# Kernel tuning notes

Hardware: AMD Instinct MI355X
Metric: run time of the kernel (lower is better)

Reference implementation:

```python
import jax, jax.numpy as jnp
import numpy as np

K = 3       # kernel size
PAD = 1     # dcn_pad
STRIDE = 1
DIL = 1     # dilation
GN_EPS = 1e-5


def _conv2d(x, w, b):
    # standard NCHW conv, stride 1, pad 1
    y = jax.lax.conv_general_dilated(
        x, w, (STRIDE, STRIDE), [(PAD, PAD), (PAD, PAD)],
        rhs_dilation=(DIL, DIL),
        dimension_numbers=('NCHW', 'OIHW', 'NCHW'))
    return y + b[None, :, None, None]


def _modulated_deform_conv(x, w_off, b_off, w, b):
    B, C, H, W = x.shape
    KK = K * K
    # offset/mask branch (ModulatedDeformConv2dPack.conv_offset)
    off = _conv2d(x, w_off, b_off)                     # [B, 3*KK, H, W]
    o1, o2, m = jnp.split(off, 3, axis=1)
    offset = jnp.concatenate([o1, o2], axis=1)         # [B, 2*KK, H, W]
    mask = jax.nn.sigmoid(m)                           # [B, KK, H, W]
    # channel 2k = dy, channel 2k+1 = dx for kernel tap k
    offset = offset.reshape(B, KK, 2, H, W)
    dy, dx = offset[:, :, 0], offset[:, :, 1]          # [B, KK, H, W]

    ki = jnp.arange(KK) // K                            # kernel row index
    kj = jnp.arange(KK) % K                             # kernel col index
    base_y = (jnp.arange(H)[None, :, None] - PAD + ki[:, None, None] * DIL)  # [KK,H,1]
    base_x = (jnp.arange(W)[None, None, :] - PAD + kj[:, None, None] * DIL)  # [KK,1,W]
    py = base_y.astype(x.dtype) + dy                   # [B, KK, H, W]
    px = base_x.astype(x.dtype) + dx

    y0f = jnp.floor(py); x0f = jnp.floor(px)
    ly = py - y0f; lx = px - x0f
    y0 = y0f.astype(jnp.int32); x0 = x0f.astype(jnp.int32)

    xf = x.reshape(B, C, H * W)

    def gather(yi, xi):
        # zero-padded gather at integer corner (yi, xi)
        valid = (yi >= 0) & (yi < H) & (xi >= 0) & (xi < W)
        idx = jnp.clip(yi, 0, H - 1) * W + jnp.clip(xi, 0, W - 1)  # [B,KK,H,W]
        g = jax.vmap(lambda xb, ib: jnp.take(xb, ib.reshape(-1), axis=1))(xf, idx)
        g = g.reshape(B, C, KK, H, W)
        return g * valid[:, None].astype(x.dtype)

    val = (gather(y0, x0)         * ((1 - ly) * (1 - lx))[:, None]
         + gather(y0, x0 + 1)     * ((1 - ly) * lx)[:, None]
         + gather(y0 + 1, x0)     * (ly * (1 - lx))[:, None]
         + gather(y0 + 1, x0 + 1) * (ly * lx)[:, None])     # [B,C,KK,H,W]
    val = val * mask[:, None]                                # modulation

    out = jnp.einsum('bckhw,ock->bohw', val, w.reshape(w.shape[0], C, KK))
    return out + b[None, :, None, None]


def _groupnorm1_relu(y, gamma, beta):
    # GroupNorm(num_groups=1): normalize over (C,H,W) per sample
    mu = y.mean(axis=(1, 2, 3), keepdims=True)
    var = y.var(axis=(1, 2, 3), keepdims=True)
    yn = (y - mu) * jax.lax.rsqrt(var + GN_EPS)
    return jax.nn.relu(yn * gamma[None, :, None, None] + beta[None, :, None, None])


def setup_inputs() -> dict:
    key = jax.random.key(0)
    ks = jax.random.split(key, 5)
    B, C, H, W = 4, 256, 64, 64
    CO = 256
    x = jax.random.normal(ks[0], (B, C, H, W), jnp.float32)
    w_off = jax.random.normal(ks[1], (3 * K * K, C, K, K), jnp.float32) * 0.01
    b_off = jax.random.normal(ks[2], (3 * K * K,), jnp.float32) * 0.01
    w = jax.random.normal(ks[3], (CO, C, K, K), jnp.float32) * (1.0 / np.sqrt(C * K * K))
    b = jax.random.normal(ks[4], (CO,), jnp.float32) * 0.01
    gamma = jnp.ones((CO,), jnp.float32)
    beta = jnp.zeros((CO,), jnp.float32)
    return dict(x=x, w_off=w_off, b_off=b_off, w=w, b=b, gamma=gamma, beta=beta)


def reference(x, w_off, b_off, w, b, gamma, beta):
    y = _modulated_deform_conv(x, w_off, b_off, w, b)
    return _groupnorm1_relu(y, gamma, beta)
```

## Files before the change

kernel.cpp:

```cpp
#include <hip/hip_runtime.h>

#define B_ 4
#define C_ 256
#define H_ 64
#define W_ 64
#define HW_ 4096
#define CO_ 256
#define NPX_ 16384
#define GN_EPS_ 1e-5f

typedef float f32x4 __attribute__((ext_vector_type(4)));
typedef short s16x8 __attribute__((ext_vector_type(8)));

__device__ __forceinline__ short f2bf(float f) {
    union { float f; unsigned u; } v; v.f = f;
    unsigned r = (v.u + 0x7FFFu + ((v.u >> 16) & 1u)) >> 16;
    return (short)(r & 0xFFFFu);
}
__device__ __forceinline__ float bf2f(short s) {
    union { unsigned u; float f; } v; v.u = ((unsigned)s & 0xFFFFu) << 16;
    return v.f;
}

__device__ __forceinline__ void gld_lds16(const void* g, void* l) {
    __builtin_amdgcn_global_load_lds(
        (const __attribute__((address_space(1))) unsigned*)g,
        (__attribute__((address_space(3))) unsigned*)l,
        16, 0, 0);
}

__global__ void k_prep_w(const float* __restrict__ w, short* __restrict__ wT) {
    int oc = blockIdx.x, c = threadIdx.x;
    const float* src = w + (oc * 256 + c) * 9;
    float v[9];
#pragma unroll
    for (int t = 0; t < 9; ++t) v[t] = src[t];
#pragma unroll
    for (int t = 0; t < 9; ++t) wT[(t * 256 + oc) * 256 + c] = f2bf(v[t]);
}

__global__ void k_prep_woff(const float* __restrict__ w_off, short* __restrict__ wOffT) {
    int o = blockIdx.x;
    int c = threadIdx.x;
    if (o < 27) {
        const float* src = w_off + (o * 256 + c) * 9;
#pragma unroll
        for (int t = 0; t < 9; ++t)
            wOffT[(t * 32 + o) * 256 + c] = f2bf(src[t]);
    } else {
#pragma unroll
        for (int t = 0; t < 9; ++t)
            wOffT[(t * 32 + o) * 256 + c] = 0;
    }
}

__global__ void k_xpose(const float* __restrict__ x, short* __restrict__ xT) {
    __shared__ short T[64 * 72];

    int bx  = blockIdx.x;
    int px0 = (bx & 255) * 64;
    int c0  = (bx >> 8) * 64;
    int b   = px0 >> 12;
    int hw0 = px0 & 4095;

    int t  = threadIdx.x;
    int cl = t & 63;
    int q  = t >> 6;

    const float4* src = reinterpret_cast<const float4*>(
        x + (long)(b * 256 + c0 + cl) * 4096 + hw0);
#pragma unroll
    for (int j = 0; j < 4; ++j) {
        float4 v = src[j * 4 + q];
        int pl = (j * 4 + q) * 4;
        T[(pl + 0) * 72 + cl] = f2bf(v.x);
        T[(pl + 1) * 72 + cl] = f2bf(v.y);
        T[(pl + 2) * 72 + cl] = f2bf(v.z);
        T[(pl + 3) * 72 + cl] = f2bf(v.w);
    }
    __syncthreads();

    int pl = t >> 2;
    int s  = t & 3;
    short* dst = xT + (long)(px0 + pl) * 256 + c0 + s * 16;
    s16x8 a    = *reinterpret_cast<const s16x8*>(&T[pl * 72 + s * 16]);
    s16x8 bseg = *reinterpret_cast<const s16x8*>(&T[pl * 72 + s * 16 + 8]);
    *reinterpret_cast<s16x8*>(dst)     = a;
    *reinterpret_cast<s16x8*>(dst + 8) = bseg;
}

__global__ __launch_bounds__(256, 4) void k_offmfma(
        const short* __restrict__ xT, const short* __restrict__ wOffT,
        const float* __restrict__ b_off, float* __restrict__ off) {
    int tid  = threadIdx.x;
    int lane = tid & 63;
    int wv   = tid >> 6;

    int px0  = blockIdx.x * 64 + wv * 16;
    int lm   = lane & 15;
    int lk   = (lane >> 4) * 8;

    int pxA = px0 + lm;
    int h   = (pxA >> 6) & 63;
    int w   = pxA & 63;

    f32x4 acc[2];
    acc[0] = (f32x4)0.f; acc[1] = (f32x4)0.f;

#pragma unroll
    for (int kk = 0; kk < 9; ++kk) {
        const int ki = kk / 3, kj = kk % 3;
        int hh = h + ki - 1, ww = w + kj - 1;
        bool valid = ((unsigned)hh < 64u) & ((unsigned)ww < 64u);
        int srcpx = valid ? (pxA + (ki - 1) * 64 + (kj - 1)) : 0;
        const short* aP = xT + (long)srcpx * 256 + lk;
        const short* bP = wOffT + (long)(kk * 32 + lm) * 256 + lk;
#pragma unroll
        for (int ks = 0; ks < 8; ++ks) {
            s16x8 a = *reinterpret_cast<const s16x8*>(aP + ks * 32);
            if (!valid) a = (s16x8)0;
            s16x8 b0 = *reinterpret_cast<const s16x8*>(bP + ks * 32);
            s16x8 b1 = *reinterpret_cast<const s16x8*>(bP + 16 * 256 + ks * 32);
            acc[0] = __builtin_amdgcn_mfma_f32_16x16x32_bf16(a, b0, acc[0], 0, 0, 0);
            acc[1] = __builtin_amdgcn_mfma_f32_16x16x32_bf16(a, b1, acc[1], 0, 0, 0);
        }
    }

#pragma unroll
    for (int nt = 0; nt < 2; ++nt) {
        int oc = nt * 16 + lm;
        if (oc < 27) {
            float bv = b_off[oc];
#pragma unroll
            for (int j = 0; j < 4; ++j) {
                int px = px0 + (lane >> 4) * 4 + j;
                off[oc * NPX_ + px] = acc[nt][j] + bv;
            }
        }
    }
}

__global__ void k_sample(const short* __restrict__ xT, const float* __restrict__ off,
                         short* __restrict__ val) {
    int tid = threadIdx.x;
    int l32 = tid & 31;
    int pxi = tid >> 5;
    int px0 = blockIdx.x * 32;

    int cb = l32 >> 2;
    int cw = (l32 & 3) * 8;

#pragma unroll 1
    for (int kk = 0; kk < 9; ++kk) {
        int ki = kk / 3, kj = kk % 3;
#pragma unroll 1
        for (int it = 0; it < 4; ++it) {
            int p  = px0 + it * 8 + pxi;
            int b  = p >> 12;
            int hw = p & 4095;
            int h  = hw >> 6;
            int wc = hw & 63;

            float dy = off[(2 * kk) * NPX_ + p];
            float dx = off[(2 * kk + 1) * NPX_ + p];
            float mk = off[(18 + kk) * NPX_ + p];
            mk = 1.f / (1.f + __expf(-mk));

            float py  = (float)(h + ki - 1) + dy;
            float pxf = (float)(wc + kj - 1) + dx;
            float y0f = floorf(py), x0f = floorf(pxf);
            float ly = py - y0f, lx = pxf - x0f;
            int y0 = (int)y0f, x0 = (int)x0f;
            int y1 = y0 + 1, x1 = x0 + 1;

            float w00 = (1.f - ly) * (1.f - lx) * mk;
            float w01 = (1.f - ly) * lx * mk;
            float w10 = ly * (1.f - lx) * mk;
            float w11 = ly * lx * mk;
            bool vy0 = (y0 >= 0) & (y0 < H_);
            bool vy1 = (y1 >= 0) & (y1 < H_);
            bool vx0 = (x0 >= 0) & (x0 < W_);
            bool vx1 = (x1 >= 0) & (x1 < W_);
            if (!(vy0 & vx0)) w00 = 0.f;
            if (!(vy0 & vx1)) w01 = 0.f;
            if (!(vy1 & vx0)) w10 = 0.f;
            if (!(vy1 & vx1)) w11 = 0.f;
            int cy0 = min(max(y0, 0), H_ - 1), cy1 = min(max(y1, 0), H_ - 1);
            int cx0 = min(max(x0, 0), W_ - 1), cx1 = min(max(x1, 0), W_ - 1);

            long rb = (long)b * 4096;
            const short* xrow = xT + l32 * 8;
            s16x8 r00 = *reinterpret_cast<const s16x8*>(xrow + (rb + cy0 * 64 + cx0) * 256);
            s16x8 r01 = *reinterpret_cast<const s16x8*>(xrow + (rb + cy0 * 64 + cx1) * 256);
            s16x8 r10 = *reinterpret_cast<const s16x8*>(xrow + (rb + cy1 * 64 + cx0) * 256);
            s16x8 r11 = *reinterpret_cast<const s16x8*>(xrow + (rb + cy1 * 64 + cx1) * 256);

            s16x8 o8;
#pragma unroll
            for (int j = 0; j < 8; ++j) {
                float g = w00 * bf2f(r00[j]) + w01 * bf2f(r01[j])
                        + w10 * bf2f(r10[j]) + w11 * bf2f(r11[j]);
                o8[j] = f2bf(g);
            }
            *reinterpret_cast<s16x8*>(val + ((long)(kk * 8 + cb) * NPX_ + p) * 32 + cw) = o8;
        }
    }
}

__global__ __launch_bounds__(512, 1) void k_gemm(
        const short* __restrict__ val, const short* __restrict__ wT,
        const float* __restrict__ bias, float* __restrict__ out,
        float* __restrict__ gnpart) {
    __shared__ char lds[65536];
    __shared__ float red[16];

    int tid  = threadIdx.x;
    int lane = tid & 63;
    int wv   = tid >> 6;

    int pxt = blockIdx.x & 127;
    int ocq = blockIdx.x >> 7;

    int px0 = pxt * 128;
    int b   = px0 >> 12;
    int hw0 = px0 & 4095;

    int wm = wv & 1;
    int wn = wv >> 1;

    int lm = lane & 15;
    int kq = lane >> 4;

    int rsub = lane >> 2;
    int qg   = (lane & 3) ^ ((lane >> 3) & 3);
    int qoff = ((kq ^ ((lane >> 1) & 3)) << 4);

    const char* valb = (const char*)val;
    const char* wTb  = (const char*)wT;

    f32x4 acc[4][2];
#pragma unroll
    for (int i = 0; i < 4; ++i)
#pragma unroll
        for (int j = 0; j < 2; ++j) acc[i][j] = (f32x4)0.f;

#define STAGE_(kidx, bufbase)                                                        \
    {                                                                                \
        int kk_ = (kidx) >> 2, cpair_ = (kidx) & 3;                                  \
        _Pragma("unroll")                                                            \
        for (int g = 0; g < 2; ++g) {                                                \
            int i_   = wv * 2 + g;                                                   \
            int R_   = i_ * 16 + rsub;                                   \
            int ksub_ = R_ >> 7;                                                     \
            int rl_   = R_ & 127;                                                    \
                                                          \
            const char* srcA = valb + ((long)((2 * (kidx) + ksub_) * NPX_            \
                               + px0 + rl_)) * 64 + qg * 16;                         \
            gld_lds16(srcA, (void*)(lds + (bufbase) + i_ * 1024));                   \
                                                          \
            const char* srcB = wTb + ((long)(kk_ * 256 + ocq * 128 + rl_)) * 512     \
                               + cpair_ * 128 + ksub_ * 64 + qg * 16;                \
            gld_lds16(srcB, (void*)(lds + (bufbase) + 16384 + i_ * 1024));           \
        }                                                                            \
    }

#define COMPUTE_(bufbase)                                                            \
    {                                                                                \
        _Pragma("unroll")                                                            \
        for (int ksub = 0; ksub < 2; ++ksub) {                                       \
            const char* Ab = lds + (bufbase) + ksub * 8192;                          \
            const char* Bb = lds + (bufbase) + 16384 + ksub * 8192;                  \
            s16x8 a[4], bf[2];                                                       \
            _Pragma("unroll")                                                        \
            for (int mf = 0; mf < 4; ++mf)                                           \
                a[mf] = *reinterpret_cast<const s16x8*>(                             \
                    Ab + (wm * 64 + mf * 16 + lm) * 64 + qoff);                      \
            _Pragma("unroll")                                                        \
            for (int nf = 0; nf < 2; ++nf)                                           \
                bf[nf] = *reinterpret_cast<const s16x8*>(                            \
                    Bb + (wn * 32 + nf * 16 + lm) * 64 + qoff);                      \
            _Pragma("unroll")                                                        \
            for (int mf = 0; mf < 4; ++mf)                                           \
                _Pragma("unroll")                                                    \
                for (int nf = 0; nf < 2; ++nf)                                       \
                    acc[mf][nf] = __builtin_amdgcn_mfma_f32_16x16x32_bf16(           \
                        a[mf], bf[nf], acc[mf][nf], 0, 0, 0);                        \
        }                                                                            \
    }

    STAGE_(0, 0);
    __syncthreads();

    int cur = 0;
#pragma unroll 1
    for (int k = 0; k < 36; ++k) {
        if (k < 35) STAGE_(k + 1, (cur ^ 1) * 32768);
        COMPUTE_(cur * 32768);
        __syncthreads();
        cur ^= 1;
    }
#undef STAGE_
#undef COMPUTE_

    float s = 0.f, sq = 0.f;
#pragma unroll
    for (int nf = 0; nf < 2; ++nf) {
        int oc = ocq * 128 + wn * 32 + nf * 16 + lm;
        float bv = bias[oc];
        float* orow = out + (b * CO_ + oc) * HW_ + hw0 + wm * 64;
#pragma unroll
        for (int mf = 0; mf < 4; ++mf) {
            f32x4 r = acc[mf][nf];
            r.x += bv; r.y += bv; r.z += bv; r.w += bv;
            s  += r.x + r.y + r.z + r.w;
            sq += r.x * r.x + r.y * r.y + r.z * r.z + r.w * r.w;
            *reinterpret_cast<f32x4*>(orow + mf * 16 + kq * 4) = r;
        }
    }
#pragma unroll
    for (int o = 32; o > 0; o >>= 1) {
        s  += __shfl_down(s, o, 64);
        sq += __shfl_down(sq, o, 64);
    }
    if (lane == 0) { red[wv * 2] = s; red[wv * 2 + 1] = sq; }
    __syncthreads();
    if (tid == 0) {
        float S = 0.f, SQ = 0.f;
#pragma unroll
        for (int k = 0; k < 8; ++k) { S += red[k * 2]; SQ += red[k * 2 + 1]; }
        gnpart[blockIdx.x * 2]     = S;
        gnpart[blockIdx.x * 2 + 1] = SQ;
    }
}

__global__ void k_gn_stats(const float* __restrict__ part, float* __restrict__ stats) {
    int b = blockIdx.x, t = threadIdx.x;
    int idx = (t >> 5) * 128 + b * 32 + (t & 31);
    float2 v = reinterpret_cast<const float2*>(part)[idx];
    float s = v.x, sq = v.y;
#pragma unroll
    for (int o = 32; o > 0; o >>= 1) {
        s  += __shfl_down(s, o, 64);
        sq += __shfl_down(sq, o, 64);
    }
    if (t == 0) {
        const float n = (float)(CO_ * HW_);
        float mean = s / n;
        float var  = sq / n - mean * mean;
        stats[b * 2] = mean;
        stats[b * 2 + 1] = rsqrtf(var + GN_EPS_);
    }
}

__global__ void k_gn_apply(float* __restrict__ y, const float* __restrict__ stats,
                           const float* __restrict__ gamma, const float* __restrict__ beta) {
    int e4 = blockIdx.x * 256 + threadIdx.x;
    int b  = e4 >> 18;
    int oc = (e4 >> 10) & 255;
    float mean = stats[b * 2], rstd = stats[b * 2 + 1];
    float g  = gamma[oc] * rstd;
    float bb = beta[oc] - mean * g;
    float4* p = reinterpret_cast<float4*>(y);
    float4 v = p[e4];
    v.x = fmaxf(v.x * g + bb, 0.f);
    v.y = fmaxf(v.y * g + bb, 0.f);
    v.z = fmaxf(v.z * g + bb, 0.f);
    v.w = fmaxf(v.w * g + bb, 0.f);
    p[e4] = v;
}

extern "C" void kernel_launch(void* const* d_in, const int* in_sizes, int n_in,
                              void* d_out, int out_size, void* d_ws, size_t ws_size,
                              hipStream_t stream) {
    const float* x     = (const float*)d_in[0];
    const float* w_off = (const float*)d_in[1];
    const float* b_off = (const float*)d_in[2];
    const float* w     = (const float*)d_in[3];
    const float* bias  = (const float*)d_in[4];
    const float* gamma = (const float*)d_in[5];
    const float* beta  = (const float*)d_in[6];
    float* out = (float*)d_out;

    float* Wp     = (float*)d_ws;
    float* off    = Wp;
    short* wT     = (short*)(off + 27 * NPX_);
    short* wOffT  = wT + 9 * 256 * 256;
    float* gnpart = (float*)(wOffT + 9 * 32 * 256);
    float* stats  = gnpart + 2048;
    short* xT     = (short*)(stats + 8);
    short* val    = xT + (long)NPX_ * 256;

    k_prep_w<<<256, 256, 0, stream>>>(w, wT);
    k_prep_woff<<<32, 256, 0, stream>>>(w_off, wOffT);
    k_xpose<<<1024, 256, 0, stream>>>(x, xT);
    k_offmfma<<<256, 256, 0, stream>>>(xT, wOffT, b_off, off);
    k_sample<<<512, 256, 0, stream>>>(xT, off, val);
    k_gemm<<<256, 512, 0, stream>>>(val, wT, bias, out, gnpart);
    k_gn_stats<<<4, 64, 0, stream>>>(gnpart, stats);
    k_gn_apply<<<4096, 256, 0, stream>>>(out, stats, gamma, beta);
}
```

Measured before the change: 196.9 us.

## Fuse bilinear sampling into deform GEMM and split-K the offset conv

The bilinear sampling stage is folded into the main GEMM. Each block computes sampled bf16 activations for 64 pixels straight into LDS and consumes them with MFMA across all 256 output channels, so the large intermediate val buffer in global memory is no longer written and read back. Separately, the offset convolution is split four ways over input channels to raise parallelism, and a small reduction kernel adds the partials and the bias. The trade-offs are one extra launch and partial buffer, sampling gathers sitting on the GEMM pipeline's critical path, and GEMM tiles reshaped to 64 px × 256 oc, which changes reuse and occupancy.

```diff
diff --git a/kernel.cpp b/kernel.cpp
--- a/kernel.cpp
+++ b/kernel.cpp
@@ -91,14 +91,15 @@
 
 __global__ __launch_bounds__(256, 4) void k_offmfma(
         const short* __restrict__ xT, const short* __restrict__ wOffT,
-        const float* __restrict__ b_off, float* __restrict__ off) {
+        float* __restrict__ offp) {
     int tid  = threadIdx.x;
     int lane = tid & 63;
     int wv   = tid >> 6;
 
     int px0  = blockIdx.x * 64 + wv * 16;
+    int cc0  = blockIdx.y * 64;
     int lm   = lane & 15;
-    int lk   = (lane >> 4) * 8;
+    int lk   = cc0 + (lane >> 4) * 8;
 
     int pxA = px0 + lm;
     int h   = (pxA >> 6) & 63;
@@ -116,7 +117,7 @@
         const short* aP = xT + (long)srcpx * 256 + lk;
         const short* bP = wOffT + (long)(kk * 32 + lm) * 256 + lk;
 #pragma unroll
-        for (int ks = 0; ks < 8; ++ks) {
+        for (int ks = 0; ks < 2; ++ks) {
             s16x8 a = *reinterpret_cast<const s16x8*>(aP + ks * 32);
             if (!valid) a = (s16x8)0;
             s16x8 b0 = *reinterpret_cast<const s16x8*>(bP + ks * 32);
@@ -126,165 +127,154 @@
         }
     }
 
+    float* op = offp + (long)blockIdx.y * 27 * NPX_;
 #pragma unroll
     for (int nt = 0; nt < 2; ++nt) {
         int oc = nt * 16 + lm;
         if (oc < 27) {
-            float bv = b_off[oc];
 #pragma unroll
             for (int j = 0; j < 4; ++j) {
                 int px = px0 + (lane >> 4) * 4 + j;
-                off[oc * NPX_ + px] = acc[nt][j] + bv;
+                op[oc * NPX_ + px] = acc[nt][j];
             }
         }
     }
 }
 
-__global__ void k_sample(const short* __restrict__ xT, const float* __restrict__ off,
-                         short* __restrict__ val) {
-    int tid = threadIdx.x;
-    int l32 = tid & 31;
-    int pxi = tid >> 5;
-    int px0 = blockIdx.x * 32;
-
-    int cb = l32 >> 2;
-    int cw = (l32 & 3) * 8;
-
-#pragma unroll 1
-    for (int kk = 0; kk < 9; ++kk) {
-        int ki = kk / 3, kj = kk % 3;
-#pragma unroll 1
-        for (int it = 0; it < 4; ++it) {
-            int p  = px0 + it * 8 + pxi;
-            int b  = p >> 12;
-            int hw = p & 4095;
-            int h  = hw >> 6;
-            int wc = hw & 63;
-
-            float dy = off[(2 * kk) * NPX_ + p];
-            float dx = off[(2 * kk + 1) * NPX_ + p];
-            float mk = off[(18 + kk) * NPX_ + p];
-            mk = 1.f / (1.f + __expf(-mk));
-
-            float py  = (float)(h + ki - 1) + dy;
-            float pxf = (float)(wc + kj - 1) + dx;
-            float y0f = floorf(py), x0f = floorf(pxf);
-            float ly = py - y0f, lx = pxf - x0f;
-            int y0 = (int)y0f, x0 = (int)x0f;
-            int y1 = y0 + 1, x1 = x0 + 1;
-
-            float w00 = (1.f - ly) * (1.f - lx) * mk;
-            float w01 = (1.f - ly) * lx * mk;
-            float w10 = ly * (1.f - lx) * mk;
-            float w11 = ly * lx * mk;
-            bool vy0 = (y0 >= 0) & (y0 < H_);
-            bool vy1 = (y1 >= 0) & (y1 < H_);
-            bool vx0 = (x0 >= 0) & (x0 < W_);
-            bool vx1 = (x1 >= 0) & (x1 < W_);
-            if (!(vy0 & vx0)) w00 = 0.f;
-            if (!(vy0 & vx1)) w01 = 0.f;
-            if (!(vy1 & vx0)) w10 = 0.f;
-            if (!(vy1 & vx1)) w11 = 0.f;
-            int cy0 = min(max(y0, 0), H_ - 1), cy1 = min(max(y1, 0), H_ - 1);
-            int cx0 = min(max(x0, 0), W_ - 1), cx1 = min(max(x1, 0), W_ - 1);
-
-            long rb = (long)b * 4096;
-            const short* xrow = xT + l32 * 8;
-            s16x8 r00 = *reinterpret_cast<const s16x8*>(xrow + (rb + cy0 * 64 + cx0) * 256);
-            s16x8 r01 = *reinterpret_cast<const s16x8*>(xrow + (rb + cy0 * 64 + cx1) * 256);
-            s16x8 r10 = *reinterpret_cast<const s16x8*>(xrow + (rb + cy1 * 64 + cx0) * 256);
-            s16x8 r11 = *reinterpret_cast<const s16x8*>(xrow + (rb + cy1 * 64 + cx1) * 256);
-
-            s16x8 o8;
-#pragma unroll
-            for (int j = 0; j < 8; ++j) {
-                float g = w00 * bf2f(r00[j]) + w01 * bf2f(r01[j])
-                        + w10 * bf2f(r10[j]) + w11 * bf2f(r11[j]);
-                o8[j] = f2bf(g);
-            }
-            *reinterpret_cast<s16x8*>(val + ((long)(kk * 8 + cb) * NPX_ + p) * 32 + cw) = o8;
-        }
-    }
-}
-
-__global__ __launch_bounds__(512, 1) void k_gemm(
-        const short* __restrict__ val, const short* __restrict__ wT,
-        const float* __restrict__ bias, float* __restrict__ out,
-        float* __restrict__ gnpart) {
-    __shared__ char lds[65536];
+__global__ void k_offreduce(const float* __restrict__ offp, const float* __restrict__ b_off,
+                            float* __restrict__ off) {
+    int idx = blockIdx.x * 256 + threadIdx.x;
+    int oc  = idx >> 14;
+    float s = b_off[oc];
+#pragma unroll
+    for (int j = 0; j < 4; ++j) s += offp[(long)j * 27 * NPX_ + idx];
+    off[idx] = s;
+}
+
+__global__ __launch_bounds__(512, 1) void k_fused(
+        const short* __restrict__ xT, const float* __restrict__ off,
+        const short* __restrict__ wT, const float* __restrict__ bias,
+        float* __restrict__ out, float* __restrict__ gnpart) {
+    __shared__ __attribute__((aligned(16))) char lds[81920];
     __shared__ float red[16];
 
     int tid  = threadIdx.x;
     int lane = tid & 63;
     int wv   = tid >> 6;
 
-    int pxt = blockIdx.x & 127;
-    int ocq = blockIdx.x >> 7;
-
-    int px0 = pxt * 128;
+    int px0 = blockIdx.x * 64;
     int b   = px0 >> 12;
     int hw0 = px0 & 4095;
-
-    int wm = wv & 1;
-    int wn = wv >> 1;
-
+    int h   = hw0 >> 6;
+    long rb = (long)b * 4096;
+
+    int spx = tid >> 3;
+    int j8  = (tid & 7) * 8;
+    int pg  = px0 + spx;
+    int abyte = spx * 128 + (((tid & 7) << 4) ^ ((spx & 7) << 4));
+
+    int brow_lane = lane >> 3;
+    int bqg = (((lane & 7) ^ brow_lane) & 7) << 4;
+
+    int wm = (wv & 1) * 32;
+    int wn = (wv >> 1) * 64;
     int lm = lane & 15;
     int kq = lane >> 4;
 
-    int rsub = lane >> 2;
-    int qg   = (lane & 3) ^ ((lane >> 3) & 3);
-    int qoff = ((kq ^ ((lane >> 1) & 3)) << 4);
-
-    const char* valb = (const char*)val;
-    const char* wTb  = (const char*)wT;
-
-    f32x4 acc[4][2];
-#pragma unroll
-    for (int i = 0; i < 4; ++i)
-#pragma unroll
-        for (int j = 0; j < 2; ++j) acc[i][j] = (f32x4)0.f;
-
-#define STAGE_(kidx, bufbase)                                                        \
+    const char* wTb = (const char*)wT;
+
+    f32x4 acc[2][4];
+#pragma unroll
+    for (int i = 0; i < 2; ++i)
+#pragma unroll
+        for (int j = 0; j < 4; ++j) acc[i][j] = (f32x4)0.f;
+
+    float sw00 = 0.f, sw01 = 0.f, sw10 = 0.f, sw11 = 0.f;
+    const short *p00 = xT, *p01 = xT, *p10 = xT, *p11 = xT;
+
+#define STAGE_(t, buf)                                                               \
     {                                                                                \
-        int kk_ = (kidx) >> 2, cpair_ = (kidx) & 3;                                  \
+        int kk_ = (t) >> 2, cq_ = (t) & 3;                                           \
+        if (((t) & 3) == 0) {                                                        \
+            int ki_ = kk_ / 3, kj_ = kk_ % 3;                                        \
+            float dy = off[(2 * kk_) * NPX_ + pg];                                   \
+            float dx = off[(2 * kk_ + 1) * NPX_ + pg];                               \
+            float mk = off[(18 + kk_) * NPX_ + pg];                                  \
+            mk = 1.f / (1.f + __expf(-mk));                                          \
+            float py  = (float)(h + ki_ - 1) + dy;                                   \
+            float pxf = (float)(spx + kj_ - 1) + dx;                                 \
+            float y0f = floorf(py), x0f = floorf(pxf);                               \
+            float ly = py - y0f, lx = pxf - x0f;                                     \
+            int y0 = (int)y0f, x0 = (int)x0f;                                        \
+            int y1 = y0 + 1, x1 = x0 + 1;                                            \
+            sw00 = (1.f - ly) * (1.f - lx) * mk;                                     \
+            sw01 = (1.f - ly) * lx * mk;                                             \
+            sw10 = ly * (1.f - lx) * mk;                                             \
+            sw11 = ly * lx * mk;                                                     \
+            bool vy0 = (y0 >= 0) & (y0 < H_);                                        \
+            bool vy1 = (y1 >= 0) & (y1 < H_);                                        \
+            bool vx0 = (x0 >= 0) & (x0 < W_);                                        \
+            bool vx1 = (x1 >= 0) & (x1 < W_);                                        \
+            if (!(vy0 & vx0)) sw00 = 0.f;                                            \
+            if (!(vy0 & vx1)) sw01 = 0.f;                                            \
+            if (!(vy1 & vx0)) sw10 = 0.f;                                            \
+            if (!(vy1 & vx1)) sw11 = 0.f;                                            \
+            int cy0 = min(max(y0, 0), H_ - 1), cy1 = min(max(y1, 0), H_ - 1);        \
+            int cx0 = min(max(x0, 0), W_ - 1), cx1 = min(max(x1, 0), W_ - 1);        \
+            p00 = xT + (rb + cy0 * 64 + cx0) * 256;                                  \
+            p01 = xT + (rb + cy0 * 64 + cx1) * 256;                                  \
+            p10 = xT + (rb + cy1 * 64 + cx0) * 256;                                  \
+            p11 = xT + (rb + cy1 * 64 + cx1) * 256;                                  \
+        }                                                                            \
         _Pragma("unroll")                                                            \
-        for (int g = 0; g < 2; ++g) {                                                \
-            int i_   = wv * 2 + g;                                                   \
-            int R_   = i_ * 16 + rsub;                                   \
-            int ksub_ = R_ >> 7;                                                     \
-            int rl_   = R_ & 127;                                                    \
-                                                          \
-            const char* srcA = valb + ((long)((2 * (kidx) + ksub_) * NPX_            \
-                               + px0 + rl_)) * 64 + qg * 16;                         \
-            gld_lds16(srcA, (void*)(lds + (bufbase) + i_ * 1024));                   \
-                                                          \
-            const char* srcB = wTb + ((long)(kk_ * 256 + ocq * 128 + rl_)) * 512     \
-                               + cpair_ * 128 + ksub_ * 64 + qg * 16;                \
-            gld_lds16(srcB, (void*)(lds + (bufbase) + 16384 + i_ * 1024));           \
+        for (int g = 0; g < 4; ++g) {                                                \
+            int row8 = wv * 4 + g;                         \
+            int ocr  = row8 * 8 + brow_lane;                                         \
+            const char* srcB = wTb + ((long)(kk_ * 256 + ocr) << 9)                  \
+                               + cq_ * 128 + bqg;                                    \
+            gld_lds16(srcB, (void*)(lds + (buf) * 40960 + 8192 + row8 * 1024));      \
         }                                                                            \
-    }
-
-#define COMPUTE_(bufbase)                                                            \
+        int coff = cq_ * 64 + j8;                                                    \
+        s16x8 r00 = *reinterpret_cast<const s16x8*>(p00 + coff);                     \
+        s16x8 r01 = *reinterpret_cast<const s16x8*>(p01 + coff);                     \
+        s16x8 r10 = *reinterpret_cast<const s16x8*>(p10 + coff);                     \
+        s16x8 r11 = *reinterpret_cast<const s16x8*>(p11 + coff);                     \
+        s16x8 o8;                                                                    \
+        _Pragma("unroll")                                                            \
+        for (int jj = 0; jj < 8; ++jj) {                                             \
+            float g2 = sw00 * bf2f(r00[jj]) + sw01 * bf2f(r01[jj])                   \
+                     + sw10 * bf2f(r10[jj]) + sw11 * bf2f(r11[jj]);                  \
+            o8[jj] = f2bf(g2);                                                       \
+        }                                                                            \
+        *reinterpret_cast<s16x8*>(lds + (buf) * 40960 + abyte) = o8;                 \
+    }
+
+#define COMPUTE_(buf)                                                                \
     {                                                                                \
+        const char* Ab = lds + (buf) * 40960;                                        \
+        const char* Bb = lds + (buf) * 40960 + 8192;                                 \
         _Pragma("unroll")                                                            \
         for (int ksub = 0; ksub < 2; ++ksub) {                                       \
-            const char* Ab = lds + (bufbase) + ksub * 8192;                          \
-            const char* Bb = lds + (bufbase) + 16384 + ksub * 8192;                  \
-            s16x8 a[4], bf[2];                                                       \
+            int cb_ = ksub * 64 + kq * 16;                                           \
+            s16x8 a[2], bfr[4];                                                      \
             _Pragma("unroll")                                                        \
-            for (int mf = 0; mf < 4; ++mf)                                           \
+            for (int mf = 0; mf < 2; ++mf) {                                         \
+                int pl_ = wm + mf * 16 + lm;                                         \
                 a[mf] = *reinterpret_cast<const s16x8*>(                             \
-                    Ab + (wm * 64 + mf * 16 + lm) * 64 + qoff);                      \
+                    Ab + pl_ * 128 + (cb_ ^ ((pl_ & 7) << 4)));                      \
+            }                                                                        \
             _Pragma("unroll")                                                        \
-            for (int nf = 0; nf < 2; ++nf)                                           \
-                bf[nf] = *reinterpret_cast<const s16x8*>(                            \
-                    Bb + (wn * 32 + nf * 16 + lm) * 64 + qoff);                      \
+            for (int nf = 0; nf < 4; ++nf) {                                         \
+                int ol_ = wn + nf * 16 + lm;                                         \
+                bfr[nf] = *reinterpret_cast<const s16x8*>(                           \
+                    Bb + ol_ * 128 + (cb_ ^ ((ol_ & 7) << 4)));                      \
+            }                                                                        \
             _Pragma("unroll")                                                        \
-            for (int mf = 0; mf < 4; ++mf)                                           \
+            for (int mf = 0; mf < 2; ++mf)                                           \
                 _Pragma("unroll")                                                    \
-                for (int nf = 0; nf < 2; ++nf)                                       \
+                for (int nf = 0; nf < 4; ++nf)                                       \
                     acc[mf][nf] = __builtin_amdgcn_mfma_f32_16x16x32_bf16(           \
-                        a[mf], bf[nf], acc[mf][nf], 0, 0, 0);                        \
+                        a[mf], bfr[nf], acc[mf][nf], 0, 0, 0);                       \
         }                                                                            \
     }
 
@@ -293,9 +283,9 @@
 
     int cur = 0;
 #pragma unroll 1
-    for (int k = 0; k < 36; ++k) {
-        if (k < 35) STAGE_(k + 1, (cur ^ 1) * 32768);
-        COMPUTE_(cur * 32768);
+    for (int t = 0; t < 36; ++t) {
+        if (t < 35) STAGE_(t + 1, cur ^ 1);
+        COMPUTE_(cur);
         __syncthreads();
         cur ^= 1;
     }
@@ -304,12 +294,12 @@
 
     float s = 0.f, sq = 0.f;
 #pragma unroll
-    for (int nf = 0; nf < 2; ++nf) {
-        int oc = ocq * 128 + wn * 32 + nf * 16 + lm;
+    for (int nf = 0; nf < 4; ++nf) {
+        int oc = wn + nf * 16 + lm;
         float bv = bias[oc];
-        float* orow = out + (b * CO_ + oc) * HW_ + hw0 + wm * 64;
-#pragma unroll
-        for (int mf = 0; mf < 4; ++mf) {
+        float* orow = out + (b * CO_ + oc) * HW_ + hw0 + wm;
+#pragma unroll
+        for (int mf = 0; mf < 2; ++mf) {
             f32x4 r = acc[mf][nf];
             r.x += bv; r.y += bv; r.z += bv; r.w += bv;
             s  += r.x + r.y + r.z + r.w;
@@ -335,8 +325,7 @@
 
 __global__ void k_gn_stats(const float* __restrict__ part, float* __restrict__ stats) {
     int b = blockIdx.x, t = threadIdx.x;
-    int idx = (t >> 5) * 128 + b * 32 + (t & 31);
-    float2 v = reinterpret_cast<const float2*>(part)[idx];
+    float2 v = reinterpret_cast<const float2*>(part)[b * 64 + t];
     float s = v.x, sq = v.y;
 #pragma unroll
     for (int o = 32; o > 0; o >>= 1) {
@@ -386,16 +375,16 @@
     short* wT     = (short*)(off + 27 * NPX_);
     short* wOffT  = wT + 9 * 256 * 256;
     float* gnpart = (float*)(wOffT + 9 * 32 * 256);
-    float* stats  = gnpart + 2048;
+    float* stats  = gnpart + 512;
     short* xT     = (short*)(stats + 8);
-    short* val    = xT + (long)NPX_ * 256;
+    float* offp   = (float*)(xT + (long)NPX_ * 256);
 
     k_prep_w<<<256, 256, 0, stream>>>(w, wT);
     k_prep_woff<<<32, 256, 0, stream>>>(w_off, wOffT);
     k_xpose<<<1024, 256, 0, stream>>>(x, xT);
-    k_offmfma<<<256, 256, 0, stream>>>(xT, wOffT, b_off, off);
-    k_sample<<<512, 256, 0, stream>>>(xT, off, val);
-    k_gemm<<<256, 512, 0, stream>>>(val, wT, bias, out, gnpart);
+    k_offmfma<<<dim3(256, 4), 256, 0, stream>>>(xT, wOffT, offp);
+    k_offreduce<<<1728, 256, 0, stream>>>(offp, b_off, off);
+    k_fused<<<256, 512, 0, stream>>>(xT, off, wT, bias, out, gnpart);
     k_gn_stats<<<4, 64, 0, stream>>>(gnpart, stats);
     k_gn_apply<<<4096, 256, 0, stream>>>(out, stats, gamma, beta);
 }
```

New measurement: 178.9 us. 9.2% less time.
